# Kernel optimization log

Hardware: AMD Instinct MI355X
Metric: run time of the kernel (lower is better)

Reference implementation:

```python
import jax, jax.numpy as jnp
import numpy as np

B, P, K, S, FLR = 128, 256, 20, 4, 64
DIMS = [(8, 256), (256, 256), (256, 512), (512, 512), (512, 512), (512, 1024), (1024, 1024), (1024, 1024)]
TOTAL_HIDDEN = 8 + sum(o for _, o in DIMS)  # 5128
HID2 = 512  # hidden_channels * 2
NB_OUT = 128


def setup_inputs() -> dict:
    key = jax.random.key(0)
    ks = iter(jax.random.split(key, 40))
    d = {}
    d["x"] = jax.random.normal(next(ks), (B * P, 8), jnp.float32)
    d["batch"] = jnp.repeat(jnp.arange(B), P)  # equal-size graphs, sorted batch ids
    for i, (fi, fo) in enumerate(DIMS):
        d[f"Ws_{i}"] = jax.random.normal(next(ks), (fi, S), jnp.float32) / float(np.sqrt(fi))
        d[f"bs_{i}"] = jnp.zeros((S,), jnp.float32)
        d[f"Wh_{i}"] = jax.random.normal(next(ks), (fi, FLR), jnp.float32) / float(np.sqrt(fi))
        d[f"bh_{i}"] = jnp.zeros((FLR,), jnp.float32)
        d[f"Wo_{i}"] = jax.random.normal(next(ks), (fi + 2 * FLR, fo), jnp.float32) / float(np.sqrt(fi + 2 * FLR))
        d[f"bo_{i}"] = jnp.zeros((fo,), jnp.float32)
    d["W_mid"] = jax.random.normal(next(ks), (TOTAL_HIDDEN, HID2), jnp.float32) / float(np.sqrt(TOTAL_HIDDEN))
    d["b_mid"] = jnp.zeros((HID2,), jnp.float32)
    d["W_head"] = jax.random.normal(next(ks), (6 * HID2, NB_OUT), jnp.float32) / float(np.sqrt(6 * HID2))
    d["b_head"] = jnp.zeros((NB_OUT,), jnp.float32)
    return d


def gravnet_conv(x, Ws, bs, Wh, bh, Wo, bo):
    # x: [B, P, Fin]. Learned coords s, propagate feats h, kNN in s-space per graph.
    s = x @ Ws + bs                      # [B, P, S]
    h = x @ Wh + bh                      # [B, P, FLR]
    sq = jnp.sum(s * s, axis=-1)         # [B, P]
    d2 = sq[:, :, None] + sq[:, None, :] - 2.0 * jnp.einsum('bpd,bqd->bpq', s, s)
    neg_d2, idx = jax.lax.top_k(-d2, K)  # k nearest neighbors (includes self)
    w = jnp.exp(-10.0 * jnp.maximum(-neg_d2, 0.0))[..., None]  # [B, P, K, 1]
    neigh = jax.vmap(lambda hb, ib: hb[ib])(h, idx)            # [B, P, K, FLR]
    m = neigh * w
    agg = jnp.concatenate([m.mean(axis=2), m.max(axis=2)], axis=-1)  # mean + max aggr
    return jnp.concatenate([x, agg], axis=-1) @ Wo + bo


def multi_pool(x):
    # x: [B, P, F]; order matches MultiAggregation(['min','max','mean','sum','std','median'])
    mean = x.mean(axis=1)
    var = (x * x).mean(axis=1) - mean * mean
    std = jnp.sqrt(jnp.clip(var, 0.0) + 1e-5)
    med = jnp.sort(x, axis=1)[:, (P - 1) // 2]  # q=0.5, 'lower' interpolation (PyG median)
    return jnp.concatenate([x.min(axis=1), x.max(axis=1), mean, x.sum(axis=1), std, med], axis=-1)


def reference(x, batch, Ws_0, bs_0, Wh_0, bh_0, Wo_0, bo_0, Ws_1, bs_1, Wh_1, bh_1, Wo_1, bo_1, Ws_2, bs_2, Wh_2, bh_2, Wo_2, bo_2, Ws_3, bs_3, Wh_3, bh_3, Wo_3, bo_3, Ws_4, bs_4, Wh_4, bh_4, Wo_4, bo_4, Ws_5, bs_5, Wh_5, bh_5, Wo_5, bo_5, Ws_6, bs_6, Wh_6, bh_6, Wo_6, bo_6, Ws_7, bs_7, Wh_7, bh_7, Wo_7, bo_7, W_mid, b_mid, W_head, b_head):
    blocks = [
        (Ws_0, bs_0, Wh_0, bh_0, Wo_0, bo_0), (Ws_1, bs_1, Wh_1, bh_1, Wo_1, bo_1),
        (Ws_2, bs_2, Wh_2, bh_2, Wo_2, bo_2), (Ws_3, bs_3, Wh_3, bh_3, Wo_3, bo_3),
        (Ws_4, bs_4, Wh_4, bh_4, Wo_4, bo_4), (Ws_5, bs_5, Wh_5, bh_5, Wo_5, bo_5),
        (Ws_6, bs_6, Wh_6, bh_6, Wo_6, bo_6), (Ws_7, bs_7, Wh_7, bh_7, Wo_7, bo_7),
    ]
    xb = x.reshape(B, P, -1)
    feats = [xb]
    for prm in blocks:
        xb = jax.nn.relu(gravnet_conv(xb, *prm))
        feats.append(xb)
    cat = jnp.concatenate(feats, axis=-1)   # [B, P, 5128]
    mid = cat @ W_mid + b_mid               # [B, P, 512]
    return multi_pool(mid) @ W_head + b_head  # [B, 128]
```

## Files before the change

### kernel.cpp

```cpp
#include <hip/hip_runtime.h>
#include <hip/hip_bf16.h>
#include <math.h>

#define M_ROWS 32768
#define GB 128
#define GP 256

typedef __hip_bfloat16 bf16;
typedef __attribute__((ext_vector_type(8))) short short8;
typedef __attribute__((ext_vector_type(4))) float f32x4;

__global__ void diag_kernel(float* out, float v) { out[0] = v; }

template<int MODE>
__global__ __launch_bounds__(256) void mgemm(
    const bf16* __restrict__ A, int lda,
    const bf16* __restrict__ Wt,
    const float* __restrict__ bias,
    float* __restrict__ out0, int ldc,
    float* __restrict__ out1,
    int K)
{
    __shared__ unsigned short Alds[128][64];
    __shared__ unsigned short Blds[128][64];
    const int tid = threadIdx.x;
    const int l = tid & 63;
    const int w = tid >> 6;
    const int wr = w >> 1, wc = w & 1;
    const int rowBase = blockIdx.x * 128;
    const int colBase = blockIdx.y * 128;

    const int lr = l >> 3;
    const int lc = (l & 7) * 8;
    const bf16* Ab = A  + (size_t)(rowBase + w * 32 + lr) * lda + lc;
    const bf16* Bb = Wt + (size_t)(colBase + w * 32 + lr) * K   + lc;

    f32x4 acc[4][4];
    #pragma unroll
    for (int m = 0; m < 4; ++m)
        #pragma unroll
        for (int n = 0; n < 4; ++n)
            acc[m][n] = (f32x4){0.f, 0.f, 0.f, 0.f};

    const int nt = K >> 6;
    for (int t = 0; t < nt; ++t) {
        const int kt = t << 6;
        __syncthreads();
        #pragma unroll
        for (int j = 0; j < 4; ++j) {
            __builtin_amdgcn_global_load_lds(
                (const __attribute__((address_space(1))) void*)(Ab + (size_t)(j * 8) * lda + kt),
                (__attribute__((address_space(3))) void*)&Alds[w * 32 + j * 8][0],
                16, 0, 0);
            __builtin_amdgcn_global_load_lds(
                (const __attribute__((address_space(1))) void*)(Bb + (size_t)(j * 8) * K + kt),
                (__attribute__((address_space(3))) void*)&Blds[w * 32 + j * 8][0],
                16, 0, 0);
        }
        __syncthreads();
        #pragma unroll
        for (int kk = 0; kk < 2; ++kk) {
            const int co = kk * 32 + (l >> 4) * 8;
            short8 a[4], b[4];
            #pragma unroll
            for (int m = 0; m < 4; ++m)
                a[m] = *(const short8*)&Alds[wr * 64 + m * 16 + (l & 15)][co];
            #pragma unroll
            for (int n = 0; n < 4; ++n)
                b[n] = *(const short8*)&Blds[wc * 64 + n * 16 + (l & 15)][co];
            #pragma unroll
            for (int m = 0; m < 4; ++m)
                #pragma unroll
                for (int n = 0; n < 4; ++n)
                    acc[m][n] = __builtin_amdgcn_mfma_f32_16x16x32_bf16(
                        a[m], b[n], acc[m][n], 0, 0, 0);
        }
    }

    const int r0 = rowBase + wr * 64 + (l >> 4) * 4;
    const int c0 = colBase + wc * 64 + (l & 15);
    #pragma unroll
    for (int m = 0; m < 4; ++m) {
        #pragma unroll
        for (int n = 0; n < 4; ++n) {
            const int col = c0 + n * 16;
            const float bv = (MODE == 2) ? 0.f : bias[col];
            #pragma unroll
            for (int g = 0; g < 4; ++g) {
                const int row = r0 + m * 16 + g;
                float v = acc[m][n][g] + bv;
                if (MODE == 0) {
                    if (col < 64)
                        ((bf16*)out0)[(size_t)row * 64 + col] = __float2bfloat16(v);
                    else if (col < 72)
                        out1[(size_t)row * 8 + (col - 64)] = v;
                } else if (MODE == 1) {
                    ((bf16*)out0)[(size_t)row * ldc + col] =
                        __float2bfloat16(fmaxf(v, 0.f));
                } else {
                    out0[(size_t)row * ldc + col] += v;
                }
            }
        }
    }
}

__global__ __launch_bounds__(256) void wprep_t(
    const float* __restrict__ W, bf16* __restrict__ Wt,
    int K, int N, int Kpad)
{
    __shared__ float tl[32][33];
    const int tx = threadIdx.x, ty = threadIdx.y;
    const int k_t = blockIdx.x * 32, n_t = blockIdx.y * 32;
    #pragma unroll
    for (int j = 0; j < 4; ++j) {
        int k = k_t + ty + j * 8;
        tl[ty + j * 8][tx] = (k < K) ? W[(size_t)k * N + n_t + tx] : 0.f;
    }
    __syncthreads();
    #pragma unroll
    for (int j = 0; j < 4; ++j) {
        int n = n_t + ty + j * 8;
        Wt[(size_t)n * Kpad + k_t + tx] = __float2bfloat16(tl[tx][ty + j * 8]);
    }
}

__global__ __launch_bounds__(256) void wprep_mid_all(
    const float* __restrict__ W_mid, bf16* __restrict__ wtm0)
{
    const int segBlkStart[10] = {0, 2, 10, 18, 34, 50, 66, 98, 130, 162};
    const int segKm[9]   = {64, 256, 256, 512, 512, 512, 1024, 1024, 1024};
    const int segKr[9]   = {8, 256, 256, 512, 512, 512, 1024, 1024, 1024};
    const int segMrow[9] = {0, 8, 264, 520, 1032, 1544, 2056, 3080, 4104};
    const int segWOff[9] = {0, 32768, 163840, 294912, 557056, 819200,
                            1081344, 1605632, 2129920};
    __shared__ float tl[32][33];
    int bx = blockIdx.x;
    int seg = 0;
    while (bx >= segBlkStart[seg + 1]) ++seg;
    const int kb = bx - segBlkStart[seg];
    const float* W = W_mid + (size_t)segMrow[seg] * 512;
    bf16* Wt = wtm0 + segWOff[seg];
    const int K = segKr[seg], Kpad = segKm[seg];
    const int tx = threadIdx.x, ty = threadIdx.y;
    const int k_t = kb * 32, n_t = blockIdx.y * 32;
    #pragma unroll
    for (int j = 0; j < 4; ++j) {
        int k = k_t + ty + j * 8;
        tl[ty + j * 8][tx] = (k < K) ? W[(size_t)k * 512 + n_t + tx] : 0.f;
    }
    __syncthreads();
    #pragma unroll
    for (int j = 0; j < 4; ++j) {
        int n = n_t + ty + j * 8;
        Wt[(size_t)n * Kpad + k_t + tx] = __float2bfloat16(tl[tx][ty + j * 8]);
    }
}

__global__ __launch_bounds__(256) void wprep_sh(
    const float* __restrict__ Wh,
    const float* __restrict__ Ws,
    bf16* __restrict__ Wt,
    int fi, int Khpad)
{
    const int k = blockIdx.x * 256 + threadIdx.x;
    const int n = blockIdx.y;
    if (k >= Khpad) return;
    float v = 0.f;
    if (k < fi) {
        if (n < 64) v = Wh[(size_t)k * 64 + n];
        else if (n < 68) {
            v = __bfloat162float(__float2bfloat16(Ws[(size_t)k * 4 + (n - 64)]));
        } else if (n < 72) {
            float wv = Ws[(size_t)k * 4 + (n - 68)];
            float hi = __bfloat162float(__float2bfloat16(wv));
            v = wv - hi;
        }
    }
    Wt[(size_t)n * Khpad + k] = __float2bfloat16(v);
}

struct BiasArgs { const float* bh[8]; const float* bs[8]; };
__global__ __launch_bounds__(128) void bias_build_all(
    BiasArgs a, float* __restrict__ out)
{
    const int L = blockIdx.x, t = threadIdx.x;
    out[L * 128 + t] = (t < 64) ? a.bh[L][t] : (t < 68 ? a.bs[L][t - 64] : 0.f);
}

__global__ __launch_bounds__(256) void f2b_pad(const float* __restrict__ in,
                                               bf16* __restrict__ out)
{
    int i = blockIdx.x * 256 + threadIdx.x;
    int row = i >> 3, c = i & 7;
    out[(size_t)row * 192 + c] = __float2bfloat16(in[i]);
}

__global__ __launch_bounds__(256) void knn_kernel(
    const float* __restrict__ sbuf,
    int* __restrict__ idx,
    float* __restrict__ wgt)
{
    __shared__ float ss[GP][5];
    const int t = threadIdx.x;
    const int b = blockIdx.x >> 6;
    {
        const float4 v1 = ((const float4*)(sbuf + ((size_t)b * GP + t) * 8))[0];
        const float4 v2 = ((const float4*)(sbuf + ((size_t)b * GP + t) * 8))[1];
        float ax = v1.x + v2.x, ay = v1.y + v2.y,
              az = v1.z + v2.z, aw = v1.w + v2.w;
        ss[t][0] = ax; ss[t][1] = ay; ss[t][2] = az; ss[t][3] = aw;
        ss[t][4] = ax * ax + ay * ay + az * az + aw * aw;
    }
    __syncthreads();

    const int w = t >> 6, l = t & 63;
    const int p = (blockIdx.x * 4 + w) & 255;
    const float px = ss[p][0], py = ss[p][1], pz = ss[p][2], pq = ss[p][3];
    const float psq = ss[p][4];

    float d0, d1, d2, d3; int q0, q1, q2, q3;
    #define KNN_DIST(DD, QQ, J) { \
        const int q_ = l + (J) * 64; \
        float dot_ = px * ss[q_][0] + py * ss[q_][1] \
                   + pz * ss[q_][2] + pq * ss[q_][3]; \
        DD = psq + ss[q_][4] - 2.f * dot_; QQ = q_; }
    KNN_DIST(d0, q0, 0) KNN_DIST(d1, q1, 1)
    KNN_DIST(d2, q2, 2) KNN_DIST(d3, q3, 3)
    #undef KNN_DIST
    #define KNN_CE(DA, DB, QA, QB) { \
        if (DA > DB) { float td = DA; DA = DB; DB = td; \
                       int tq = QA; QA = QB; QB = tq; } }
    KNN_CE(d0, d1, q0, q1) KNN_CE(d2, d3, q2, q3)
    KNN_CE(d0, d2, q0, q2) KNN_CE(d1, d3, q1, q3)
    KNN_CE(d1, d2, q1, q2)
    #undef KNN_CE

    const size_t base = ((size_t)b * GP + p) * 20;
    #pragma unroll
    for (int k = 0; k < 20; ++k) {
        float m = d0;
        #pragma unroll
        for (int off = 32; off; off >>= 1)
            m = fminf(m, __shfl_xor(m, off));
        unsigned long long msk = __ballot(d0 == m);
        int winner = __ffsll((long long)msk) - 1;
        if (l == winner) {
            idx[base + k] = q0;
            wgt[base + k] = expf(-10.f * fmaxf(m, 0.f));
            d0 = d1; q0 = q1; d1 = d2; q1 = q2;
            d2 = d3; q2 = q3; d3 = 3.402823466e38f;
        }
    }
}

__global__ __launch_bounds__(256) void gather_kernel(
    const bf16* __restrict__ h,
    const int* __restrict__ idx,
    const float* __restrict__ wgt,
    bf16* __restrict__ xtgt, int stride, int fiL, int padN)
{
    const int t = threadIdx.x;
    const int f = t & 63;
    const int lp = t >> 6;
    const int pt = blockIdx.x * 4 + lp;
    const int b = pt >> 8;
    const size_t base = (size_t)pt * 20;
    float sum = 0.f, mx = -3.402823466e38f;
    for (int k = 0; k < 20; ++k) {
        int q = idx[base + k];
        float wv = wgt[base + k];
        float val = __bfloat162float(h[(((size_t)b << 8) + q) * 64 + f]) * wv;
        sum += val;
        mx = fmaxf(mx, val);
    }
    bf16* out = xtgt + (size_t)pt * stride + fiL;
    out[f] = __float2bfloat16(sum * (1.f / 20.f));
    out[64 + f] = __float2bfloat16(mx);
    if (f < padN) out[128 + f] = __float2bfloat16(0.f);
}

__global__ __launch_bounds__(256) void init_mid(float* __restrict__ mid,
                                                const float* __restrict__ b_mid)
{
    size_t i = (size_t)blockIdx.x * 256 + threadIdx.x;
    mid[i] = b_mid[i & 511];
}

__global__ __launch_bounds__(256) void pool_kernel(
    const float* __restrict__ mid,
    float* __restrict__ pooled)
{
    __shared__ float tile[GP][33];
    __shared__ float rbuf[256];
    const int b = blockIdx.x;
    const int c0 = blockIdx.y * 32;
    const int t = threadIdx.x;

    #pragma unroll 8
    for (int l = 0; l < 32; ++l) {
        int lin = l * 256 + t;
        int row = lin >> 5;
        int col = lin & 31;
        tile[row][col] = mid[((size_t)b * GP + row) * 512 + c0 + col];
    }
    __syncthreads();

    const int col = t & 31, g = t >> 5;
    float mn = 3.402823466e38f, mx = -3.402823466e38f, sm = 0.f, s2 = 0.f;
    for (int r = g * 32; r < g * 32 + 32; ++r) {
        float v = tile[r][col];
        mn = fminf(mn, v); mx = fmaxf(mx, v); sm += v; s2 += v * v;
    }
    float* outb = pooled + (size_t)b * 3072 + c0;

    rbuf[t] = mn; __syncthreads();
    if (t < 32) {
        float v = rbuf[t];
        #pragma unroll
        for (int k = 1; k < 8; ++k) v = fminf(v, rbuf[t + 32 * k]);
        outb[0 * 512 + t] = v;
    }
    __syncthreads();
    rbuf[t] = mx; __syncthreads();
    if (t < 32) {
        float v = rbuf[t];
        #pragma unroll
        for (int k = 1; k < 8; ++k) v = fmaxf(v, rbuf[t + 32 * k]);
        outb[1 * 512 + t] = v;
    }
    __syncthreads();
    rbuf[t] = sm; __syncthreads();
    float meanv = 0.f;
    if (t < 32) {
        float v = 0.f;
        #pragma unroll
        for (int k = 0; k < 8; ++k) v += rbuf[t + 32 * k];
        meanv = v * (1.f / 256.f);
        outb[2 * 512 + t] = meanv;
        outb[3 * 512 + t] = v;
    }
    __syncthreads();
    rbuf[t] = s2; __syncthreads();
    if (t < 32) {
        float v = 0.f;
        #pragma unroll
        for (int k = 0; k < 8; ++k) v += rbuf[t + 32 * k];
        float var = v * (1.f / 256.f) - meanv * meanv;
        outb[4 * 512 + t] = sqrtf(fmaxf(var, 0.f) + 1e-5f);
    }

    for (int size = 2; size <= 256; size <<= 1) {
        for (int stride = size >> 1; stride > 0; stride >>= 1) {
            __syncthreads();
            #pragma unroll
            for (int it = 0; it < 16; ++it) {
                int task = it * 256 + t;
                int c = task & 31;
                int pp = task >> 5;
                int i = 2 * pp - (pp & (stride - 1));
                int j = i + stride;
                bool up = ((i & size) == 0);
                float va = tile[i][c], vb = tile[j][c];
                bool sw = up ? (va > vb) : (va < vb);
                if (sw) { tile[i][c] = vb; tile[j][c] = va; }
            }
        }
    }
    __syncthreads();
    if (t < 32) outb[5 * 512 + t] = tile[127][t];
}

__global__ __launch_bounds__(128) void head_kernel(
    const float* __restrict__ pooled,
    const float* __restrict__ Wh,
    const float* __restrict__ bh,
    float* __restrict__ out)
{
    __shared__ float sh[3072];
    const int b = blockIdx.x, t = threadIdx.x;
    for (int l = t; l < 3072; l += 128) sh[l] = pooled[(size_t)b * 3072 + l];
    __syncthreads();
    float acc = bh[t];
    for (int k = 0; k < 3072; ++k) acc += sh[k] * Wh[(size_t)k * 128 + t];
    out[(size_t)b * 128 + t] = acc;
}

extern "C" void kernel_launch(void* const* d_in, const int* in_sizes, int n_in,
                              void* d_out, int out_size, void* d_ws, size_t ws_size,
                              hipStream_t stream)
{
    const int fi[8] = {8, 256, 256, 512, 512, 512, 1024, 1024};
    const int fo[8] = {256, 256, 512, 512, 512, 1024, 1024, 1024};
    const int Kh[8] = {64, 256, 256, 512, 512, 512, 1024, 1024};
    const int Ko[8] = {192, 384, 384, 640, 640, 640, 1152, 1152};
    const int Km[9] = {64, 256, 256, 512, 512, 512, 1024, 1024, 1024};
    const int S[9]  = {192, 384, 384, 640, 640, 640, 1152, 1152, 1024};

    const float* x      = (const float*)d_in[0];
    const float* W_mid  = (const float*)d_in[50];
    const float* b_mid  = (const float*)d_in[51];
    const float* W_head = (const float*)d_in[52];
    const float* b_head = (const float*)d_in[53];

    const size_t M = M_ROWS;

    char* p = (char*)d_ws;
    float* mid    = (float*)p; p += M * 512 * 4;
    float* sbuf   = (float*)p; p += M * 8 * 4;
    float* pooled = (float*)p; p += 128 * 3072 * 4;
    float* wgtb   = (float*)p; p += M * 20 * 4;
    int*   idxb   = (int*)p;   p += M * 20 * 4;
    bf16*  hbuf   = (bf16*)p;  p += M * 64 * 2;
    bf16*  xA     = (bf16*)p;  p += M * 1152 * 2;
    bf16*  xB     = (bf16*)p;  p += M * 1152 * 2;
    float* biassh = (float*)p; p += 8 * 128 * 4;
    bf16*  wpool  = (bf16*)p;
    bf16* wsh[8]; bf16* wto[8]; bf16* wtm[9];
    {
        bf16* wp = wpool;
        for (int L = 0; L < 8; ++L) { wsh[L] = wp; wp += (size_t)128 * Kh[L]; }
        for (int L = 0; L < 8; ++L) { wto[L] = wp; wp += (size_t)fo[L] * Ko[L]; }
        for (int i = 0; i < 9; ++i) { wtm[i] = wp; wp += (size_t)512 * Km[i]; }
        p = (char*)wp;
    }
    size_t needed = (size_t)(p - (char*)d_ws);
    if (ws_size < needed) {
        diag_kernel<<<1, 1, 0, stream>>>((float*)d_out, (float)ws_size);
        return;
    }

    BiasArgs ba;
    for (int L = 0; L < 8; ++L) {
        const float* Ws = (const float*)d_in[2 + 6 * L];
        const float* bs = (const float*)d_in[3 + 6 * L];
        const float* Wh = (const float*)d_in[4 + 6 * L];
        const float* bh = (const float*)d_in[5 + 6 * L];
        const float* Wo = (const float*)d_in[6 + 6 * L];
        ba.bh[L] = bh; ba.bs[L] = bs;
        wprep_sh<<<dim3((Kh[L] + 255) / 256, 128), 256, 0, stream>>>(
            Wh, Ws, wsh[L], fi[L], Kh[L]);
        wprep_t<<<dim3(Ko[L] / 32, fo[L] / 32), dim3(32, 8), 0, stream>>>(
            Wo, wto[L], fi[L] + 128, fo[L], Ko[L]);
    }
    bias_build_all<<<8, 128, 0, stream>>>(ba, biassh);
    wprep_mid_all<<<dim3(162, 16), dim3(32, 8), 0, stream>>>(W_mid, wtm[0]);

    f2b_pad<<<(int)(M * 8 / 256), 256, 0, stream>>>(x, xA);
    init_mid<<<(int)(M * 512 / 256), 256, 0, stream>>>(mid, b_mid);

    bf16* bufs[2] = {xA, xB};
    for (int L = 0; L < 8; ++L) {
        bf16* xin = bufs[L & 1];
        bf16* xout = bufs[(L + 1) & 1];
        const float* bo = (const float*)d_in[7 + 6 * L];

        mgemm<0><<<dim3(256, 1), 256, 0, stream>>>(
            xin, S[L], wsh[L], biassh + L * 128, (float*)hbuf, 64, sbuf, Kh[L]);
        knn_kernel<<<(int)(M / 4), 256, 0, stream>>>(sbuf, idxb, wgtb);
        gather_kernel<<<(int)(M / 4), 256, 0, stream>>>(
            hbuf, idxb, wgtb, xin, S[L], fi[L], (L == 0) ? 56 : 0);
        mgemm<2><<<dim3(256, 4), 256, 0, stream>>>(
            xin, S[L], wtm[L], nullptr, mid, 512, nullptr, Km[L]);
        mgemm<1><<<dim3(256, fo[L] / 128), 256, 0, stream>>>(
            xin, S[L], wto[L], bo, (float*)xout, S[L + 1], nullptr, Ko[L]);
    }
    mgemm<2><<<dim3(256, 4), 256, 0, stream>>>(
        bufs[0], S[8], wtm[8], nullptr, mid, 512, nullptr, Km[8]);

    pool_kernel<<<dim3(GB, 16), 256, 0, stream>>>(mid, pooled);
    head_kernel<<<GB, 128, 0, stream>>>(pooled, W_head, b_head, (float*)d_out);
}
```

Measured before the change: 2.172 ms.

## Store all layer features in one wide buffer and do a single mid GEMM

When the workspace is large enough, every layer's bf16 output goes into one concatenated feature buffer of width 5184. The nine accumulating mid-GEMMs and init_mid are replaced by one K=5184 GEMM that writes directly with the bias. The GEMM gains a two-source A operand so the output projection reads the layer input and a separate aggregation buffer, with the Wo rows remapped to match. The kNN selection loop is also rewritten to use a DPP integer min-reduce, readlane and a single batched store, and clamps distances before selecting. This trades a larger workspace and extra branching for fewer read-modify-write passes over the fp32 mid buffer and fewer launches.

```diff
diff --git a/kernel.cpp b/kernel.cpp
--- a/kernel.cpp
+++ b/kernel.cpp
@@ -14,7 +14,8 @@
 
 template<int MODE>
 __global__ __launch_bounds__(256) void mgemm(
-    const bf16* __restrict__ A, int lda,
+    const bf16* __restrict__ A1, int lda1,
+    const bf16* __restrict__ A2, int lda2, int splitTile,
     const bf16* __restrict__ Wt,
     const float* __restrict__ bias,
     float* __restrict__ out0, int ldc,
@@ -32,8 +33,10 @@
 
     const int lr = l >> 3;
     const int lc = (l & 7) * 8;
-    const bf16* Ab = A  + (size_t)(rowBase + w * 32 + lr) * lda + lc;
-    const bf16* Bb = Wt + (size_t)(colBase + w * 32 + lr) * K   + lc;
+    const int arow = rowBase + w * 32 + lr;
+    const bf16* A1b = A1 + (size_t)arow * lda1 + lc;
+    const bf16* A2b = A2 ? (A2 + (size_t)arow * lda2 + lc) : A1b;
+    const bf16* Bb  = Wt + (size_t)(colBase + w * 32 + lr) * K + lc;
 
     f32x4 acc[4][4];
     #pragma unroll
@@ -44,16 +47,19 @@
 
     const int nt = K >> 6;
     for (int t = 0; t < nt; ++t) {
-        const int kt = t << 6;
+        const bf16* bp; int ldsel; int ko;
+        if (t < splitTile) { bp = A1b; ldsel = lda1; ko = t << 6; }
+        else               { bp = A2b; ldsel = lda2; ko = (t - splitTile) << 6; }
+        const int kb = t << 6;
         __syncthreads();
         #pragma unroll
         for (int j = 0; j < 4; ++j) {
             __builtin_amdgcn_global_load_lds(
-                (const __attribute__((address_space(1))) void*)(Ab + (size_t)(j * 8) * lda + kt),
+                (const __attribute__((address_space(1))) void*)(bp + (size_t)(j * 8) * ldsel + ko),
                 (__attribute__((address_space(3))) void*)&Alds[w * 32 + j * 8][0],
                 16, 0, 0);
             __builtin_amdgcn_global_load_lds(
-                (const __attribute__((address_space(1))) void*)(Bb + (size_t)(j * 8) * K + kt),
+                (const __attribute__((address_space(1))) void*)(Bb + (size_t)(j * 8) * K + kb),
                 (__attribute__((address_space(3))) void*)&Blds[w * 32 + j * 8][0],
                 16, 0, 0);
         }
@@ -97,8 +103,10 @@
                 } else if (MODE == 1) {
                     ((bf16*)out0)[(size_t)row * ldc + col] =
                         __float2bfloat16(fmaxf(v, 0.f));
+                } else if (MODE == 2) {
+                    out0[(size_t)row * ldc + col] += v;
                 } else {
-                    out0[(size_t)row * ldc + col] += v;
+                    out0[(size_t)row * ldc + col] = v;
                 }
             }
         }
@@ -107,7 +115,7 @@
 
 __global__ __launch_bounds__(256) void wprep_t(
     const float* __restrict__ W, bf16* __restrict__ Wt,
-    int K, int N, int Kpad)
+    int fiReal, int fiPad, int N, int Kpad)
 {
     __shared__ float tl[32][33];
     const int tx = threadIdx.x, ty = threadIdx.y;
@@ -115,7 +123,10 @@
     #pragma unroll
     for (int j = 0; j < 4; ++j) {
         int k = k_t + ty + j * 8;
-        tl[ty + j * 8][tx] = (k < K) ? W[(size_t)k * N + n_t + tx] : 0.f;
+        int s = (k < fiReal) ? k : ((k >= fiPad) ? (k - fiPad + fiReal) : -1);
+        float v = 0.f;
+        if (s >= 0 && s < fiReal + 128) v = W[(size_t)s * N + n_t + tx];
+        tl[ty + j * 8][tx] = v;
     }
     __syncthreads();
     #pragma unroll
@@ -157,11 +168,35 @@
     }
 }
 
+__global__ __launch_bounds__(256) void wprep_mid_big(
+    const float* __restrict__ W_mid, bf16* __restrict__ Wt)
+{
+    const int off_[9]  = {0, 64, 320, 576, 1088, 1600, 2112, 3136, 4160};
+    const int size_[9] = {8, 256, 256, 512, 512, 512, 1024, 1024, 1024};
+    const int mrow_[9] = {0, 8, 264, 520, 1032, 1544, 2056, 3080, 4104};
+    __shared__ float tl[32][33];
+    const int tx = threadIdx.x, ty = threadIdx.y;
+    const int k_t = blockIdx.x * 32, n_t = blockIdx.y * 32;
+    #pragma unroll
+    for (int j = 0; j < 4; ++j) {
+        int k = k_t + ty + j * 8;
+        int s = -1;
+        #pragma unroll
+        for (int g = 0; g < 9; ++g)
+            if (k >= off_[g] && k < off_[g] + size_[g]) s = mrow_[g] + (k - off_[g]);
+        tl[ty + j * 8][tx] = (s >= 0) ? W_mid[(size_t)s * 512 + n_t + tx] : 0.f;
+    }
+    __syncthreads();
+    #pragma unroll
+    for (int j = 0; j < 4; ++j) {
+        int n = n_t + ty + j * 8;
+        Wt[(size_t)n * 5184 + k_t + tx] = __float2bfloat16(tl[tx][ty + j * 8]);
+    }
+}
+
 __global__ __launch_bounds__(256) void wprep_sh(
-    const float* __restrict__ Wh,
-    const float* __restrict__ Ws,
-    bf16* __restrict__ Wt,
-    int fi, int Khpad)
+    const float* __restrict__ Wh, const float* __restrict__ Ws,
+    bf16* __restrict__ Wt, int fi, int Khpad)
 {
     const int k = blockIdx.x * 256 + threadIdx.x;
     const int n = blockIdx.y;
@@ -196,6 +231,27 @@
     out[(size_t)row * 192 + c] = __float2bfloat16(in[i]);
 }
 
+__global__ __launch_bounds__(256) void f2b_big(const float* __restrict__ in,
+                                               bf16* __restrict__ feat)
+{
+    int i = blockIdx.x * 256 + threadIdx.x;
+    int row = i >> 6, c = i & 63;
+    feat[(size_t)row * 5184 + c] =
+        __float2bfloat16(c < 8 ? in[row * 8 + c] : 0.f);
+}
+
+__device__ __forceinline__ int wave_imin_bcast(int x)
+{
+    int y;
+    y = __builtin_amdgcn_update_dpp(x, x, 0x111, 0xf, 0xf, false); x = y < x ? y : x;
+    y = __builtin_amdgcn_update_dpp(x, x, 0x112, 0xf, 0xf, false); x = y < x ? y : x;
+    y = __builtin_amdgcn_update_dpp(x, x, 0x114, 0xf, 0xf, false); x = y < x ? y : x;
+    y = __builtin_amdgcn_update_dpp(x, x, 0x118, 0xf, 0xf, false); x = y < x ? y : x;
+    y = __builtin_amdgcn_update_dpp(x, x, 0x142, 0xf, 0xf, false); x = y < x ? y : x;
+    y = __builtin_amdgcn_update_dpp(x, x, 0x143, 0xf, 0xf, false); x = y < x ? y : x;
+    return __builtin_amdgcn_readlane(x, 63);
+}
+
 __global__ __launch_bounds__(256) void knn_kernel(
     const float* __restrict__ sbuf,
     int* __restrict__ idx,
@@ -224,7 +280,7 @@
         const int q_ = l + (J) * 64; \
         float dot_ = px * ss[q_][0] + py * ss[q_][1] \
                    + pz * ss[q_][2] + pq * ss[q_][3]; \
-        DD = psq + ss[q_][4] - 2.f * dot_; QQ = q_; }
+        DD = fmaxf(psq + ss[q_][4] - 2.f * dot_, 0.f); QQ = q_; }
     KNN_DIST(d0, q0, 0) KNN_DIST(d1, q1, 1)
     KNN_DIST(d2, q2, 2) KNN_DIST(d3, q3, 3)
     #undef KNN_DIST
@@ -236,27 +292,29 @@
     KNN_CE(d1, d2, q1, q2)
     #undef KNN_CE
 
-    const size_t base = ((size_t)b * GP + p) * 20;
+    float outd = 0.f; int outq = 0;
     #pragma unroll
     for (int k = 0; k < 20; ++k) {
-        float m = d0;
-        #pragma unroll
-        for (int off = 32; off; off >>= 1)
-            m = fminf(m, __shfl_xor(m, off));
-        unsigned long long msk = __ballot(d0 == m);
-        int winner = __ffsll((long long)msk) - 1;
-        if (l == winner) {
-            idx[base + k] = q0;
-            wgt[base + k] = expf(-10.f * fmaxf(m, 0.f));
-            d0 = d1; q0 = q1; d1 = d2; q1 = q2;
-            d2 = d3; q2 = q3; d3 = 3.402823466e38f;
-        }
+        const int mb = wave_imin_bcast(__float_as_int(d0));
+        unsigned long long msk = __ballot(__float_as_int(d0) == mb);
+        const int winner = __ffsll((long long)msk) - 1;
+        const int qwin = __builtin_amdgcn_readlane(q0, winner);
+        if (l == k) { outd = __int_as_float(mb); outq = qwin; }
+        const bool pop = (l == winner);
+        d0 = pop ? d1 : d0; q0 = pop ? q1 : q0;
+        d1 = pop ? d2 : d1; q1 = pop ? q2 : q1;
+        d2 = pop ? d3 : d2; q2 = pop ? q3 : q2;
+        d3 = pop ? 3.402823466e38f : d3;
+    }
+    if (l < 20) {
+        const size_t base = ((size_t)b * GP + p) * 20;
+        idx[base + l] = outq;
+        wgt[base + l] = expf(-10.f * outd);
     }
 }
 
 __global__ __launch_bounds__(256) void gather_kernel(
-    const bf16* __restrict__ h,
-    const int* __restrict__ idx,
+    const bf16* __restrict__ h, const int* __restrict__ idx,
     const float* __restrict__ wgt,
     bf16* __restrict__ xtgt, int stride, int fiL, int padN)
 {
@@ -288,8 +346,7 @@
 }
 
 __global__ __launch_bounds__(256) void pool_kernel(
-    const float* __restrict__ mid,
-    float* __restrict__ pooled)
+    const float* __restrict__ mid, float* __restrict__ pooled)
 {
     __shared__ float tile[GP][33];
     __shared__ float rbuf[256];
@@ -372,10 +429,8 @@
 }
 
 __global__ __launch_bounds__(128) void head_kernel(
-    const float* __restrict__ pooled,
-    const float* __restrict__ Wh,
-    const float* __restrict__ bh,
-    float* __restrict__ out)
+    const float* __restrict__ pooled, const float* __restrict__ Wh,
+    const float* __restrict__ bh, float* __restrict__ out)
 {
     __shared__ float sh[3072];
     const int b = blockIdx.x, t = threadIdx.x;
@@ -390,12 +445,14 @@
                               void* d_out, int out_size, void* d_ws, size_t ws_size,
                               hipStream_t stream)
 {
-    const int fi[8] = {8, 256, 256, 512, 512, 512, 1024, 1024};
-    const int fo[8] = {256, 256, 512, 512, 512, 1024, 1024, 1024};
-    const int Kh[8] = {64, 256, 256, 512, 512, 512, 1024, 1024};
-    const int Ko[8] = {192, 384, 384, 640, 640, 640, 1152, 1152};
-    const int Km[9] = {64, 256, 256, 512, 512, 512, 1024, 1024, 1024};
-    const int S[9]  = {192, 384, 384, 640, 640, 640, 1152, 1152, 1024};
+    const int fi[8]  = {8, 256, 256, 512, 512, 512, 1024, 1024};
+    const int fip[8] = {64, 256, 256, 512, 512, 512, 1024, 1024};
+    const int fo[8]  = {256, 256, 512, 512, 512, 1024, 1024, 1024};
+    const int Kh[8]  = {64, 256, 256, 512, 512, 512, 1024, 1024};
+    const int Ko[8]  = {192, 384, 384, 640, 640, 640, 1152, 1152};
+    const int Km[9]  = {64, 256, 256, 512, 512, 512, 1024, 1024, 1024};
+    const int off[9] = {0, 64, 320, 576, 1088, 1600, 2112, 3136, 4160};
+    const int S[9]   = {192, 384, 384, 640, 640, 640, 1152, 1152, 1024};
 
     const float* x      = (const float*)d_in[0];
     const float* W_mid  = (const float*)d_in[50];
@@ -411,26 +468,64 @@
     float* pooled = (float*)p; p += 128 * 3072 * 4;
     float* wgtb   = (float*)p; p += M * 20 * 4;
     int*   idxb   = (int*)p;   p += M * 20 * 4;
+    float* biassh = (float*)p; p += 8 * 128 * 4;
     bf16*  hbuf   = (bf16*)p;  p += M * 64 * 2;
-    bf16*  xA     = (bf16*)p;  p += M * 1152 * 2;
-    bf16*  xB     = (bf16*)p;  p += M * 1152 * 2;
-    float* biassh = (float*)p; p += 8 * 128 * 4;
-    bf16*  wpool  = (bf16*)p;
-    bf16* wsh[8]; bf16* wto[8]; bf16* wtm[9];
-    {
-        bf16* wp = wpool;
-        for (int L = 0; L < 8; ++L) { wsh[L] = wp; wp += (size_t)128 * Kh[L]; }
-        for (int L = 0; L < 8; ++L) { wto[L] = wp; wp += (size_t)fo[L] * Ko[L]; }
-        for (int i = 0; i < 9; ++i) { wtm[i] = wp; wp += (size_t)512 * Km[i]; }
-        p = (char*)wp;
-    }
-    size_t needed = (size_t)(p - (char*)d_ws);
-    if (ws_size < needed) {
+
+    char* pb = p;
+    bf16* aggb = (bf16*)pb; pb += M * 128 * 2;
+    bf16* feat = (bf16*)pb; pb += M * 5184 * 2;
+    bf16* wshB = (bf16*)pb;
+    {
+        bf16* wp = wshB;
+        for (int L = 0; L < 8; ++L) wp += (size_t)128 * Kh[L];
+        pb = (char*)wp;
+    }
+    bf16* wtoB = (bf16*)pb;
+    {
+        bf16* wp = wtoB;
+        for (int L = 0; L < 8; ++L) wp += (size_t)fo[L] * Ko[L];
+        pb = (char*)wp;
+    }
+    bf16* wtmB = (bf16*)pb; pb += (size_t)512 * 5184 * 2;
+    const size_t neededBig = (size_t)(pb - (char*)d_ws);
+
+    char* ps = p;
+    bf16* xA = (bf16*)ps; ps += M * 1152 * 2;
+    bf16* xB = (bf16*)ps; ps += M * 1152 * 2;
+    bf16* wshS = (bf16*)ps;
+    {
+        bf16* wp = wshS;
+        for (int L = 0; L < 8; ++L) wp += (size_t)128 * Kh[L];
+        ps = (char*)wp;
+    }
+    bf16* wtoS = (bf16*)ps;
+    {
+        bf16* wp = wtoS;
+        for (int L = 0; L < 8; ++L) wp += (size_t)fo[L] * Ko[L];
+        ps = (char*)wp;
+    }
+    bf16* wtmS = (bf16*)ps;
+    {
+        bf16* wp = wtmS;
+        for (int i = 0; i < 9; ++i) wp += (size_t)512 * Km[i];
+        ps = (char*)wp;
+    }
+    const size_t neededSmall = (size_t)(ps - (char*)d_ws);
+
+    if (ws_size < neededSmall) {
         diag_kernel<<<1, 1, 0, stream>>>((float*)d_out, (float)ws_size);
         return;
     }
+    const bool big = (ws_size >= neededBig);
 
     BiasArgs ba;
+    bf16* wsh[8]; bf16* wto[8];
+    {
+        bf16* wp = big ? wshB : wshS;
+        for (int L = 0; L < 8; ++L) { wsh[L] = wp; wp += (size_t)128 * Kh[L]; }
+        wp = big ? wtoB : wtoS;
+        for (int L = 0; L < 8; ++L) { wto[L] = wp; wp += (size_t)fo[L] * Ko[L]; }
+    }
     for (int L = 0; L < 8; ++L) {
         const float* Ws = (const float*)d_in[2 + 6 * L];
         const float* bs = (const float*)d_in[3 + 6 * L];
@@ -441,32 +536,61 @@
         wprep_sh<<<dim3((Kh[L] + 255) / 256, 128), 256, 0, stream>>>(
             Wh, Ws, wsh[L], fi[L], Kh[L]);
         wprep_t<<<dim3(Ko[L] / 32, fo[L] / 32), dim3(32, 8), 0, stream>>>(
-            Wo, wto[L], fi[L] + 128, fo[L], Ko[L]);
+            Wo, wto[L], fi[L], big ? fip[L] : fi[L], fo[L], Ko[L]);
     }
     bias_build_all<<<8, 128, 0, stream>>>(ba, biassh);
-    wprep_mid_all<<<dim3(162, 16), dim3(32, 8), 0, stream>>>(W_mid, wtm[0]);
-
-    f2b_pad<<<(int)(M * 8 / 256), 256, 0, stream>>>(x, xA);
-    init_mid<<<(int)(M * 512 / 256), 256, 0, stream>>>(mid, b_mid);
-
-    bf16* bufs[2] = {xA, xB};
-    for (int L = 0; L < 8; ++L) {
-        bf16* xin = bufs[L & 1];
-        bf16* xout = bufs[(L + 1) & 1];
-        const float* bo = (const float*)d_in[7 + 6 * L];
-
-        mgemm<0><<<dim3(256, 1), 256, 0, stream>>>(
-            xin, S[L], wsh[L], biassh + L * 128, (float*)hbuf, 64, sbuf, Kh[L]);
-        knn_kernel<<<(int)(M / 4), 256, 0, stream>>>(sbuf, idxb, wgtb);
-        gather_kernel<<<(int)(M / 4), 256, 0, stream>>>(
-            hbuf, idxb, wgtb, xin, S[L], fi[L], (L == 0) ? 56 : 0);
+
+    if (big) {
+        wprep_mid_big<<<dim3(162, 16), dim3(32, 8), 0, stream>>>(W_mid, wtmB);
+        f2b_big<<<(int)(M * 64 / 256), 256, 0, stream>>>(x, feat);
+
+        for (int L = 0; L < 8; ++L) {
+            const float* bo = (const float*)d_in[7 + 6 * L];
+            mgemm<0><<<dim3(256, 1), 256, 0, stream>>>(
+                feat + off[L], 5184, nullptr, 0, 9999,
+                wsh[L], biassh + L * 128, (float*)hbuf, 64, sbuf, Kh[L]);
+            knn_kernel<<<(int)(M / 4), 256, 0, stream>>>(sbuf, idxb, wgtb);
+            gather_kernel<<<(int)(M / 4), 256, 0, stream>>>(
+                hbuf, idxb, wgtb, aggb, 128, 0, 0);
+            mgemm<1><<<dim3(256, fo[L] / 128), 256, 0, stream>>>(
+                feat + off[L], 5184, aggb, 128, fip[L] >> 6,
+                wto[L], bo, (float*)(feat + off[L + 1]), 5184, nullptr, Ko[L]);
+        }
+        mgemm<3><<<dim3(256, 4), 256, 0, stream>>>(
+            feat, 5184, nullptr, 0, 9999,
+            wtmB, b_mid, mid, 512, nullptr, 5184);
+    } else {
+        bf16* wtm[9];
+        {
+            bf16* wp = wtmS;
+            for (int i = 0; i < 9; ++i) { wtm[i] = wp; wp += (size_t)512 * Km[i]; }
+        }
+        wprep_mid_all<<<dim3(162, 16), dim3(32, 8), 0, stream>>>(W_mid, wtm[0]);
+        f2b_pad<<<(int)(M * 8 / 256), 256, 0, stream>>>(x, xA);
+        init_mid<<<(int)(M * 512 / 256), 256, 0, stream>>>(mid, b_mid);
+
+        bf16* bufs[2] = {xA, xB};
+        for (int L = 0; L < 8; ++L) {
+            bf16* xin = bufs[L & 1];
+            bf16* xout = bufs[(L + 1) & 1];
+            const float* bo = (const float*)d_in[7 + 6 * L];
+            mgemm<0><<<dim3(256, 1), 256, 0, stream>>>(
+                xin, S[L], nullptr, 0, 9999,
+                wsh[L], biassh + L * 128, (float*)hbuf, 64, sbuf, Kh[L]);
+            knn_kernel<<<(int)(M / 4), 256, 0, stream>>>(sbuf, idxb, wgtb);
+            gather_kernel<<<(int)(M / 4), 256, 0, stream>>>(
+                hbuf, idxb, wgtb, xin, S[L], fi[L], (L == 0) ? 56 : 0);
+            mgemm<2><<<dim3(256, 4), 256, 0, stream>>>(
+                xin, S[L], nullptr, 0, 9999,
+                wtm[L], nullptr, mid, 512, nullptr, Km[L]);
+            mgemm<1><<<dim3(256, fo[L] / 128), 256, 0, stream>>>(
+                xin, S[L], nullptr, 0, 9999,
+                wto[L], bo, (float*)xout, S[L + 1], nullptr, Ko[L]);
+        }
         mgemm<2><<<dim3(256, 4), 256, 0, stream>>>(
-            xin, S[L], wtm[L], nullptr, mid, 512, nullptr, Km[L]);
-        mgemm<1><<<dim3(256, fo[L] / 128), 256, 0, stream>>>(
-            xin, S[L], wto[L], bo, (float*)xout, S[L + 1], nullptr, Ko[L]);
-    }
-    mgemm<2><<<dim3(256, 4), 256, 0, stream>>>(
-        bufs[0], S[8], wtm[8], nullptr, mid, 512, nullptr, Km[8]);
+            bufs[0], S[8], nullptr, 0, 9999,
+            wtm[8], nullptr, mid, 512, nullptr, Km[8]);
+    }
 
     pool_kernel<<<dim3(GB, 16), 256, 0, stream>>>(mid, pooled);
     head_kernel<<<GB, 128, 0, stream>>>(pooled, W_head, b_head, (float*)d_out);
```

New measurement: 2.081 ms. 1.04x faster.
